# Optimization experiments

Measured on AMD Instinct MI355X. Metric: run time of the kernel, lower is better.

Reference implementation:

```python
import jax, jax.numpy as jnp
import numpy as np

N_NODES = 50000
N_EDGES = 600000
IN_FEAT = 128
OUT_FEAT = 128
NUM_RELS = 8


def setup_inputs() -> dict:
    key = jax.random.key(0)
    ks = jax.random.split(key, 8)
    h = jax.random.normal(ks[0], (N_NODES, IN_FEAT), dtype=jnp.float32)
    # xavier_uniform-like scale for relation weights
    limit = float(np.sqrt(6.0 / (IN_FEAT + OUT_FEAT)))
    weight = jax.random.uniform(ks[1], (NUM_RELS, IN_FEAT, OUT_FEAT), jnp.float32, -limit, limit)
    limit_g = float(np.sqrt(6.0 / (IN_FEAT + 1)))
    gate_weight = jax.random.uniform(ks[2], (NUM_RELS, IN_FEAT, 1), jnp.float32, -limit_g, limit_g)
    h_bias = jnp.zeros((OUT_FEAT,), jnp.float32)
    loop_weight = jax.random.uniform(ks[3], (IN_FEAT, OUT_FEAT), jnp.float32, -limit, limit)
    norm = jax.random.uniform(ks[4], (N_EDGES, 1), jnp.float32)
    src = jax.random.randint(ks[5], (N_EDGES,), 0, N_NODES, dtype=jnp.int32)
    dst = jax.random.randint(ks[6], (N_EDGES,), 0, N_NODES, dtype=jnp.int32)
    rel_type = jax.random.randint(ks[7], (N_EDGES,), 0, NUM_RELS, dtype=jnp.int32)
    return {"h": h, "weight": weight, "gate_weight": gate_weight, "h_bias": h_bias,
            "loop_weight": loop_weight, "norm": norm, "src": src, "dst": dst,
            "rel_type": rel_type}


def reference(h, weight, gate_weight, h_bias, loop_weight, norm, src, dst, rel_type):
    n_nodes = h.shape[0]
    # Transform all nodes under every relation once ([R, N, out]); cheaper than
    # materializing per-edge [E, in, out] weight gathers for small R.
    h_rel = jnp.einsum('ni,rio->rno', h, weight)          # [R, N, out]
    msg = h_rel[rel_type, src]                             # [E, out] gather
    msg = msg * norm                                       # per-edge norm
    # relation-specific scalar gate on src features
    gate_rel = jnp.einsum('ni,ri->rn', h, gate_weight[:, :, 0])  # [R, N]
    gate = jax.nn.sigmoid(gate_rel[rel_type, src])[:, None]      # [E, 1]
    msg = msg * gate
    # scatter-sum messages into destination nodes
    agg = jax.ops.segment_sum(msg, dst, num_segments=n_nodes)    # [N, out]
    out = agg + h_bias + h @ loop_weight                   # bias + self-loop
    out = jax.nn.relu(out)                                 # activation
    # dropout p=0.0 (deterministic) -> identity
    return out
```

## Files before the change

kernel.cpp:

```cpp
#include <hip/hip_runtime.h>

#define N_NODES 50000
#define N_EDGES 600000
#define F 128
#define NRELL 9
#define NB_SCAN 196

#define WT_OFF     0
#define WT_BYTES   (9*128*128*2)
#define GATE_OFF   294912
#define GATE_BYTES (8*N_NODES*4)
#define HREL_OFF   1894912
#define HREL_BYTES (9ll*N_NODES*128*2)
#define CNT_OFF    117094912
#define BASE_OFF   117294912
#define CUR_OFF    117494912
#define BSUM_OFF   117694912
#define SORT_OFF   117695936
#define WS_NEED2   ((size_t)120095936)
#define WS_NEED1   ((size_t)HREL_OFF + (size_t)HREL_BYTES)

typedef __attribute__((ext_vector_type(8))) short short8;
typedef __attribute__((ext_vector_type(4))) float floatx4;

__device__ inline unsigned short f32_to_bf16(float f) {
    unsigned u = __float_as_uint(f);
    unsigned r = u + 0x7fff + ((u >> 16) & 1);
    return (unsigned short)(r >> 16);
}
__device__ inline float bf16_to_f32(unsigned short s) {
    return __uint_as_float(((unsigned)s) << 16);
}
__device__ inline float sigmoidf(float x) { return 1.f / (1.f + __expf(-x)); }

__global__ void k_prep_w(const float* __restrict__ W, const float* __restrict__ LW,
                         unsigned short* __restrict__ Wt) {
    int idx = blockIdx.x * 256 + threadIdx.x;
    if (idx >= 9 * 128 * 128) return;
    int r = idx >> 14;
    int rem = idx & 16383;
    int i = rem >> 7, o = rem & 127;
    float v = (r < 8) ? W[(r << 14) + (i << 7) + o] : LW[(i << 7) + o];
    Wt[(r << 14) + (o << 7) + i] = f32_to_bf16(v);
}

__global__ void k_gate(const float* __restrict__ h, const float* __restrict__ gw,
                       float* __restrict__ gate) {
    int wave = threadIdx.x >> 6, lane = threadIdx.x & 63;
    int n = blockIdx.x * 4 + wave;
    if (n >= N_NODES) return;
    float2 hv = *(const float2*)(h + (size_t)n * F + lane * 2);
    #pragma unroll
    for (int r = 0; r < 8; ++r) {
        float2 wv = *(const float2*)(gw + r * F + lane * 2);
        float p = hv.x * wv.x + hv.y * wv.y;
        #pragma unroll
        for (int off = 32; off; off >>= 1) p += __shfl_xor(p, off);
        if (lane == 0) gate[r * N_NODES + n] = sigmoidf(p);
    }
}

#define LDH 136
#define LDW 136
__global__ __launch_bounds__(256) void k_hrel(const float* __restrict__ h,
                                              const unsigned short* __restrict__ Wt,
                                              unsigned short* __restrict__ hrel) {
    __shared__ unsigned short hA[64 * LDH];
    __shared__ unsigned short wB[128 * LDW];
    int tid = threadIdx.x;
    int nb = blockIdx.x * 64;

    #pragma unroll
    for (int it = 0; it < 8; ++it) {
        int idx = it * 1024 + tid * 4;
        int row = idx >> 7, col = idx & 127;
        int node = nb + row;
        float4 v;
        if (node < N_NODES) v = *(const float4*)(h + (size_t)node * F + col);
        else                v = make_float4(0.f, 0.f, 0.f, 0.f);
        ushort4 b;
        b.x = f32_to_bf16(v.x); b.y = f32_to_bf16(v.y);
        b.z = f32_to_bf16(v.z); b.w = f32_to_bf16(v.w);
        *(ushort4*)(&hA[row * LDH + col]) = b;
    }

    int wave = tid >> 6, lane = tid & 63;
    int lrow = lane & 15, quad = lane >> 4;
    const unsigned short* aptr = &hA[(wave * 16 + lrow) * LDH + quad * 8];

    for (int r = 0; r < NRELL; ++r) {
        __syncthreads();
        #pragma unroll
        for (int it = 0; it < 8; ++it) {
            int idx = it * 2048 + tid * 8;
            int o = idx >> 7, i = idx & 127;
            *(uint4*)(&wB[o * LDW + i]) = *(const uint4*)(Wt + (r << 14) + idx);
        }
        __syncthreads();

        floatx4 acc[8];
        #pragma unroll
        for (int nt = 0; nt < 8; ++nt) acc[nt] = (floatx4){0.f, 0.f, 0.f, 0.f};
        #pragma unroll
        for (int kt = 0; kt < 4; ++kt) {
            short8 a = *(const short8*)(aptr + kt * 32);
            #pragma unroll
            for (int nt = 0; nt < 8; ++nt) {
                short8 b = *(const short8*)(&wB[(nt * 16 + lrow) * LDW + kt * 32 + quad * 8]);
                acc[nt] = __builtin_amdgcn_mfma_f32_16x16x32_bf16(a, b, acc[nt], 0, 0, 0);
            }
        }
        unsigned short* dstp = hrel + (size_t)r * N_NODES * F;
        #pragma unroll
        for (int nt = 0; nt < 8; ++nt) {
            #pragma unroll
            for (int g = 0; g < 4; ++g) {
                int node = nb + wave * 16 + quad * 4 + g;
                if (node < N_NODES)
                    dstp[(size_t)node * F + nt * 16 + lrow] = f32_to_bf16(acc[nt][g]);
            }
        }
    }
}

__global__ void k_hist(const int* __restrict__ dst, int* __restrict__ cnt) {
    int e = blockIdx.x * 256 + threadIdx.x;
    if (e < N_EDGES) atomicAdd(&cnt[dst[e]], 1);
}

__global__ void k_scan1(const int* __restrict__ cnt, int* __restrict__ excl,
                        int* __restrict__ bsum) {
    __shared__ int sh[256];
    int g = blockIdx.x * 256 + threadIdx.x;
    int v = (g < N_NODES) ? cnt[g] : 0;
    sh[threadIdx.x] = v;
    __syncthreads();
    #pragma unroll
    for (int off = 1; off < 256; off <<= 1) {
        int t = (threadIdx.x >= off) ? sh[threadIdx.x - off] : 0;
        __syncthreads();
        sh[threadIdx.x] += t;
        __syncthreads();
    }
    if (g < N_NODES) excl[g] = sh[threadIdx.x] - v;
    if (threadIdx.x == 255) bsum[blockIdx.x] = sh[255];
}

__global__ void k_scan2(int* __restrict__ bsum) {
    __shared__ int sh[256];
    int v = (threadIdx.x < NB_SCAN) ? bsum[threadIdx.x] : 0;
    sh[threadIdx.x] = v;
    __syncthreads();
    #pragma unroll
    for (int off = 1; off < 256; off <<= 1) {
        int t = (threadIdx.x >= off) ? sh[threadIdx.x - off] : 0;
        __syncthreads();
        sh[threadIdx.x] += t;
        __syncthreads();
    }
    if (threadIdx.x < NB_SCAN) bsum[threadIdx.x] = sh[threadIdx.x] - v;
}

__global__ void k_scan3(int* __restrict__ excl, const int* __restrict__ bsum,
                        int* __restrict__ cursor) {
    int g = blockIdx.x * 256 + threadIdx.x;
    if (g < N_NODES) {
        int b = excl[g] + bsum[blockIdx.x];
        excl[g] = b;
        cursor[g] = b;
    }
}

__global__ void k_scatter(const int* __restrict__ dst, int* __restrict__ cursor,
                          int* __restrict__ sorted) {
    int e = blockIdx.x * 256 + threadIdx.x;
    if (e < N_EDGES) {
        int pos = atomicAdd(&cursor[dst[e]], 1);
        sorted[pos] = e;
    }
}

__global__ __launch_bounds__(256) void k_agg(const unsigned short* __restrict__ hrel,
                      const float* __restrict__ gate,
                      const float* __restrict__ norm,
                      const int* __restrict__ src, const int* __restrict__ rel,
                      const int* __restrict__ sorted,
                      const int* __restrict__ base, const int* __restrict__ cnt,
                      const float* __restrict__ bias,
                      float* __restrict__ out) {
    int wave = threadIdx.x >> 6, lane = threadIdx.x & 63;
    int n = blockIdx.x * 4 + wave;
    if (n >= N_NODES) return;
    int startp = base[n];
    int deg = cnt[n];
    float acc0 = 0.f, acc1 = 0.f;
    for (int c0 = 0; c0 < deg; c0 += 64) {
        int myi = c0 + lane;
        float sc = 0.f;
        int row = 0;
        if (myi < deg) {
            int e = sorted[startp + myi];
            int s = src[e], r = rel[e];
            row = r * N_NODES + s;
            sc = norm[e] * gate[row];
        }
        int lim = (deg - c0 < 64) ? (deg - c0) : 64;
        for (int i = 0; i < lim; ++i) {
            float scl = __shfl(sc, i);
            int rw = __shfl(row, i);
            unsigned m = *(const unsigned*)(hrel + (size_t)rw * F + lane * 2);
            acc0 += scl * bf16_to_f32((unsigned short)(m & 0xffffu));
            acc1 += scl * bf16_to_f32((unsigned short)(m >> 16));
        }
    }
    const unsigned short* hrel8 = hrel + (size_t)8 * N_NODES * F;
    unsigned l8 = *(const unsigned*)(hrel8 + (size_t)n * F + lane * 2);
    float2 bv = *(const float2*)(bias + lane * 2);
    float o0 = fmaxf(acc0 + bv.x + bf16_to_f32((unsigned short)(l8 & 0xffffu)), 0.f);
    float o1 = fmaxf(acc1 + bv.y + bf16_to_f32((unsigned short)(l8 >> 16)), 0.f);
    *(float2*)(out + (size_t)n * F + lane * 2) = make_float2(o0, o1);
}

__global__ void k_edges(const unsigned short* __restrict__ hrel,
                        const float* __restrict__ gate,
                        const float* __restrict__ norm,
                        const int* __restrict__ src, const int* __restrict__ dst,
                        const int* __restrict__ rel,
                        float* __restrict__ out) {
    int wave = threadIdx.x >> 6, lane = threadIdx.x & 63;
    int e = blockIdx.x * 4 + wave;
    if (e >= N_EDGES) return;
    int s = src[e], d = dst[e], r = rel[e];
    float scale = norm[e] * gate[r * N_NODES + s];
    unsigned int m = *(const unsigned int*)(hrel + ((size_t)r * N_NODES + s) * F + lane * 2);
    float v0 = bf16_to_f32((unsigned short)(m & 0xffffu)) * scale;
    float v1 = bf16_to_f32((unsigned short)(m >> 16)) * scale;
    float* op = out + (size_t)d * F + lane * 2;
    unsafeAtomicAdd(op, v0);
    unsafeAtomicAdd(op + 1, v1);
}

__global__ void k_final(float* __restrict__ out, const float* __restrict__ bias,
                        const unsigned short* __restrict__ hrel8) {
    int idx = blockIdx.x * 256 + threadIdx.x;
    if (idx >= N_NODES * 32) return;
    int node = idx >> 5, c4 = (idx & 31) * 4;
    float4 a = *(float4*)(out + (size_t)node * F + c4);
    float4 b = *(const float4*)(bias + c4);
    ushort4 l = *(const ushort4*)(hrel8 + (size_t)node * F + c4);
    float o0 = fmaxf(a.x + b.x + bf16_to_f32(l.x), 0.f);
    float o1 = fmaxf(a.y + b.y + bf16_to_f32(l.y), 0.f);
    float o2 = fmaxf(a.z + b.z + bf16_to_f32(l.z), 0.f);
    float o3 = fmaxf(a.w + b.w + bf16_to_f32(l.w), 0.f);
    *(float4*)(out + (size_t)node * F + c4) = make_float4(o0, o1, o2, o3);
}

__global__ void k_edges_fb(const float* __restrict__ h, const float* __restrict__ W,
                           const float* __restrict__ gw, const float* __restrict__ norm,
                           const int* __restrict__ src, const int* __restrict__ dst,
                           const int* __restrict__ rel, float* __restrict__ out) {
    int wave = threadIdx.x >> 6, lane = threadIdx.x & 63;
    int e = blockIdx.x * 4 + wave;
    if (e >= N_EDGES) return;
    int s = src[e], d = dst[e], r = rel[e];
    float2 hv = *(const float2*)(h + (size_t)s * F + lane * 2);
    float2 gv = *(const float2*)(gw + r * F + lane * 2);
    float p = hv.x * gv.x + hv.y * gv.y;
    #pragma unroll
    for (int off = 32; off; off >>= 1) p += __shfl_xor(p, off);
    float scale = norm[e] * sigmoidf(p);
    const float* wr = W + ((size_t)r << 14);
    float a0 = 0.f, a1 = 0.f;
    for (int i2 = 0; i2 < 64; ++i2) {
        float x0 = __shfl(hv.x, i2), x1 = __shfl(hv.y, i2);
        a0 += x0 * wr[(2 * i2) * F + lane]      + x1 * wr[(2 * i2 + 1) * F + lane];
        a1 += x0 * wr[(2 * i2) * F + 64 + lane] + x1 * wr[(2 * i2 + 1) * F + 64 + lane];
    }
    unsafeAtomicAdd(out + (size_t)d * F + lane,      a0 * scale);
    unsafeAtomicAdd(out + (size_t)d * F + 64 + lane, a1 * scale);
}

__global__ void k_final_fb(const float* __restrict__ h, const float* __restrict__ LW,
                           const float* __restrict__ bias, float* __restrict__ out) {
    int wave = threadIdx.x >> 6, lane = threadIdx.x & 63;
    int n = blockIdx.x * 4 + wave;
    if (n >= N_NODES) return;
    float2 hv = *(const float2*)(h + (size_t)n * F + lane * 2);
    float a0 = 0.f, a1 = 0.f;
    for (int i2 = 0; i2 < 64; ++i2) {
        float x0 = __shfl(hv.x, i2), x1 = __shfl(hv.y, i2);
        a0 += x0 * LW[(2 * i2) * F + lane]      + x1 * LW[(2 * i2 + 1) * F + lane];
        a1 += x0 * LW[(2 * i2) * F + 64 + lane] + x1 * LW[(2 * i2 + 1) * F + 64 + lane];
    }
    float* op = out + (size_t)n * F;
    op[lane]      = fmaxf(op[lane]      + bias[lane]      + a0, 0.f);
    op[64 + lane] = fmaxf(op[64 + lane] + bias[64 + lane] + a1, 0.f);
}

extern "C" void kernel_launch(void* const* d_in, const int* in_sizes, int n_in,
                              void* d_out, int out_size, void* d_ws, size_t ws_size,
                              hipStream_t stream) {
    const float* h    = (const float*)d_in[0];
    const float* W    = (const float*)d_in[1];
    const float* gw   = (const float*)d_in[2];
    const float* bias = (const float*)d_in[3];
    const float* lw   = (const float*)d_in[4];
    const float* norm = (const float*)d_in[5];
    const int* src    = (const int*)d_in[6];
    const int* dst    = (const int*)d_in[7];
    const int* rel    = (const int*)d_in[8];
    float* out = (float*)d_out;

    if (ws_size >= WS_NEED2) {
        unsigned short* Wt   = (unsigned short*)d_ws;
        float*          gate = (float*)((char*)d_ws + GATE_OFF);
        unsigned short* hrel = (unsigned short*)((char*)d_ws + HREL_OFF);
        int* cnt    = (int*)((char*)d_ws + CNT_OFF);
        int* base   = (int*)((char*)d_ws + BASE_OFF);
        int* cursor = (int*)((char*)d_ws + CUR_OFF);
        int* bsum   = (int*)((char*)d_ws + BSUM_OFF);
        int* sorted = (int*)((char*)d_ws + SORT_OFF);

        hipMemsetAsync(cnt, 0, N_NODES * sizeof(int), stream);
        k_prep_w<<<576, 256, 0, stream>>>(W, lw, Wt);
        k_gate<<<12500, 256, 0, stream>>>(h, gw, gate);
        k_hist<<<2344, 256, 0, stream>>>(dst, cnt);
        k_scan1<<<NB_SCAN, 256, 0, stream>>>(cnt, base, bsum);
        k_scan2<<<1, 256, 0, stream>>>(bsum);
        k_scan3<<<NB_SCAN, 256, 0, stream>>>(base, bsum, cursor);
        k_scatter<<<2344, 256, 0, stream>>>(dst, cursor, sorted);
        k_hrel<<<782, 256, 0, stream>>>(h, Wt, hrel);
        k_agg<<<12500, 256, 0, stream>>>(hrel, gate, norm, src, rel, sorted,
                                         base, cnt, bias, out);
    } else if (ws_size >= WS_NEED1) {
        unsigned short* Wt   = (unsigned short*)d_ws;
        float*          gate = (float*)((char*)d_ws + GATE_OFF);
        unsigned short* hrel = (unsigned short*)((char*)d_ws + HREL_OFF);
        hipMemsetAsync(d_out, 0, (size_t)out_size * sizeof(float), stream);
        k_prep_w<<<576, 256, 0, stream>>>(W, lw, Wt);
        k_gate<<<12500, 256, 0, stream>>>(h, gw, gate);
        k_hrel<<<782, 256, 0, stream>>>(h, Wt, hrel);
        k_edges<<<150000, 256, 0, stream>>>(hrel, gate, norm, src, dst, rel, out);
        k_final<<<6250, 256, 0, stream>>>(out, bias, hrel + (size_t)8 * N_NODES * F);
    } else {
        hipMemsetAsync(d_out, 0, (size_t)out_size * sizeof(float), stream);
        k_edges_fb<<<150000, 256, 0, stream>>>(h, W, gw, norm, src, dst, rel, out);
        k_final_fb<<<12500, 256, 0, stream>>>(h, lw, bias, out);
    }
}
```

Before: 302.4 us.

## Aggregate raw features per relation first, then one fused GEMM over concatenated relations

Reorders the computation so messages are summed per (dst, relation) from bf16 node features first, then multiplied by the stacked relation and self-loop weights in a single K=1152 MFMA GEMM with fused bias and ReLU. This avoids materialising the 9×N×128 transformed-feature tensor and the per-edge gathers from it. Edges are bucketed by dst*8+rel, with norm×gate folded into packed (src, scale) records. The new path adds an extra bf16 rounding of the aggregates, a larger scan, and depends on a workspace of about 138 MB being available.

```diff
diff --git a/kernel.cpp b/kernel.cpp
--- a/kernel.cpp
+++ b/kernel.cpp
@@ -5,11 +5,19 @@
 #define F 128
 #define NRELL 9
 #define NB_SCAN 196
-
-#define WT_OFF     0
-#define WT_BYTES   (9*128*128*2)
+#define NB2 1563
+
+#define WT3_OFF   0
+#define H2_OFF    294912
+#define GATE3_OFF 13094912
+#define CNT3_OFF  14694912
+#define EXCL3_OFF 16294912
+#define BSUM3_OFF 17895168
+#define REC3_OFF  17901568
+#define A3_OFF    22701568
+#define WS_NEED3  ((size_t)138012160)
+
 #define GATE_OFF   294912
-#define GATE_BYTES (8*N_NODES*4)
 #define HREL_OFF   1894912
 #define HREL_BYTES (9ll*N_NODES*128*2)
 #define CNT_OFF    117094912
@@ -31,17 +39,230 @@
 __device__ inline float bf16_to_f32(unsigned short s) {
     return __uint_as_float(((unsigned)s) << 16);
 }
+__device__ inline float bf16lo(unsigned m) { return __uint_as_float(m << 16); }
+__device__ inline float bf16hi(unsigned m) { return __uint_as_float(m & 0xffff0000u); }
 __device__ inline float sigmoidf(float x) { return 1.f / (1.f + __expf(-x)); }
 
 __global__ void k_prep_w(const float* __restrict__ W, const float* __restrict__ LW,
-                         unsigned short* __restrict__ Wt) {
+                         unsigned short* __restrict__ Wt, int swz) {
     int idx = blockIdx.x * 256 + threadIdx.x;
     if (idx >= 9 * 128 * 128) return;
     int r = idx >> 14;
     int rem = idx & 16383;
     int i = rem >> 7, o = rem & 127;
     float v = (r < 8) ? W[(r << 14) + (i << 7) + o] : LW[(i << 7) + o];
-    Wt[(r << 14) + (o << 7) + i] = f32_to_bf16(v);
+    int pos;
+    if (swz) {
+        int g = (i >> 3) ^ (o & 7);
+        pos = (r << 14) + (o << 7) + (g << 3) + (i & 7);
+    } else {
+        pos = (r << 14) + (o << 7) + i;
+    }
+    Wt[pos] = f32_to_bf16(v);
+}
+
+__global__ void k_prep_h(const float* __restrict__ h, const float* __restrict__ gw,
+                         unsigned short* __restrict__ h2, float* __restrict__ gate) {
+    int wave = threadIdx.x >> 6, lane = threadIdx.x & 63;
+    int n = blockIdx.x * 4 + wave;
+    float2 hv = *(const float2*)(h + (size_t)n * F + lane * 2);
+    unsigned val = (unsigned)f32_to_bf16(hv.x) | ((unsigned)f32_to_bf16(hv.y) << 16);
+    *(unsigned*)(h2 + (size_t)n * F + lane * 2) = val;
+    #pragma unroll
+    for (int r = 0; r < 8; ++r) {
+        float2 wv = *(const float2*)(gw + r * F + lane * 2);
+        float p = hv.x * wv.x + hv.y * wv.y;
+        #pragma unroll
+        for (int off = 32; off; off >>= 1) p += __shfl_xor(p, off);
+        if (lane == 0) gate[r * N_NODES + n] = sigmoidf(p);
+    }
+}
+
+__global__ void k_hist2(const int* __restrict__ dst, const int* __restrict__ rel,
+                        int* __restrict__ cnt) {
+    int e = blockIdx.x * 256 + threadIdx.x;
+    if (e < N_EDGES) atomicAdd(&cnt[dst[e] * 8 + rel[e]], 1);
+}
+
+__global__ void k_s1(const int* __restrict__ cnt, int* __restrict__ excl,
+                     int* __restrict__ bsum) {
+    __shared__ int sh[256];
+    int g = blockIdx.x * 256 + threadIdx.x;
+    int v = (g < 400000) ? cnt[g] : 0;
+    sh[threadIdx.x] = v;
+    __syncthreads();
+    #pragma unroll
+    for (int off = 1; off < 256; off <<= 1) {
+        int t = (threadIdx.x >= off) ? sh[threadIdx.x - off] : 0;
+        __syncthreads();
+        sh[threadIdx.x] += t;
+        __syncthreads();
+    }
+    if (g < 400000) excl[g] = sh[threadIdx.x] - v;
+    if (threadIdx.x == 255) bsum[blockIdx.x] = sh[255];
+}
+
+__global__ void k_s2(int* __restrict__ bsum) {
+    __shared__ int sh[256];
+    int t = threadIdx.x;
+    int v[7];
+    int s = 0;
+    #pragma unroll
+    for (int j = 0; j < 7; ++j) {
+        int idx = t * 7 + j;
+        v[j] = (idx < NB2) ? bsum[idx] : 0;
+        s += v[j];
+    }
+    sh[t] = s;
+    __syncthreads();
+    #pragma unroll
+    for (int off = 1; off < 256; off <<= 1) {
+        int tt = (t >= off) ? sh[t - off] : 0;
+        __syncthreads();
+        sh[t] += tt;
+        __syncthreads();
+    }
+    int run = sh[t] - s;
+    #pragma unroll
+    for (int j = 0; j < 7; ++j) {
+        int idx = t * 7 + j;
+        if (idx < NB2) bsum[idx] = run;
+        run += v[j];
+    }
+}
+
+__global__ void k_s3(int* __restrict__ excl, const int* __restrict__ bsum,
+                     int* __restrict__ cursor) {
+    int g = blockIdx.x * 256 + threadIdx.x;
+    if (g < 400000) {
+        int b = excl[g] + bsum[blockIdx.x];
+        excl[g] = b;
+        cursor[g] = b;
+    }
+    if (g == 0) excl[400000] = N_EDGES;
+}
+
+__global__ void k_scatter2(const int* __restrict__ src, const int* __restrict__ dst,
+                           const int* __restrict__ rel, const float* __restrict__ norm,
+                           const float* __restrict__ gate, int* __restrict__ cursor,
+                           int2* __restrict__ rec) {
+    int e = blockIdx.x * 256 + threadIdx.x;
+    if (e >= N_EDGES) return;
+    int d = dst[e], r = rel[e], s = src[e];
+    int pos = atomicAdd(&cursor[d * 8 + r], 1);
+    float sc = norm[e] * gate[r * N_NODES + s];
+    rec[pos] = make_int2(s, __float_as_int(sc));
+}
+
+__global__ __launch_bounds__(256) void k_aggA(const unsigned short* __restrict__ h2,
+                                              const int2* __restrict__ rec,
+                                              const int* __restrict__ excl,
+                                              unsigned short* __restrict__ A) {
+    int wave = threadIdx.x >> 6, lane = threadIdx.x & 63;
+    int n = blockIdx.x * 4 + wave;
+    int ex = 0;
+    if (lane < 9) ex = excl[n * 8 + lane];
+    int e0 = __shfl(ex, 0), e8 = __shfl(ex, 8);
+    int deg = e8 - e0;
+    unsigned short* Arow = A + (size_t)n * 1152;
+    int swo = (((lane >> 2) ^ (n & 7)) << 2) + (lane & 3);
+
+    if (deg <= 64) {
+        int rs = 0; float rsc = 0.f;
+        if (lane < deg) {
+            int2 rc = rec[e0 + lane];
+            rs = rc.x; rsc = __int_as_float(rc.y);
+        }
+        for (int r = 0; r < 8; ++r) {
+            int s = __shfl(ex, r) - e0;
+            int e = __shfl(ex, r + 1) - e0;
+            float a0 = 0.f, a1 = 0.f;
+            for (int j = s; j < e; ++j) {
+                int sj = __shfl(rs, j);
+                float sc = __shfl(rsc, j);
+                unsigned m = *(const unsigned*)(h2 + (size_t)sj * F + lane * 2);
+                a0 += sc * bf16lo(m);
+                a1 += sc * bf16hi(m);
+            }
+            unsigned val = (unsigned)f32_to_bf16(a0) | ((unsigned)f32_to_bf16(a1) << 16);
+            ((unsigned*)(Arow + r * 128))[swo] = val;
+        }
+    } else {
+        for (int r = 0; r < 8; ++r) {
+            int s = __shfl(ex, r);
+            int e = __shfl(ex, r + 1);
+            float a0 = 0.f, a1 = 0.f;
+            for (int idx = s; idx < e; ++idx) {
+                int2 rc = rec[idx];
+                float sc = __int_as_float(rc.y);
+                unsigned m = *(const unsigned*)(h2 + (size_t)rc.x * F + lane * 2);
+                a0 += sc * bf16lo(m);
+                a1 += sc * bf16hi(m);
+            }
+            unsigned val = (unsigned)f32_to_bf16(a0) | ((unsigned)f32_to_bf16(a1) << 16);
+            ((unsigned*)(Arow + r * 128))[swo] = val;
+        }
+    }
+    unsigned hm = ((const unsigned*)(h2 + (size_t)n * F))[lane];
+    ((unsigned*)(Arow + 8 * 128))[swo] = hm;
+}
+
+__global__ __launch_bounds__(256) void k_gemmA(const unsigned short* __restrict__ A,
+                                               const unsigned short* __restrict__ Wt,
+                                               const float* __restrict__ bias,
+                                               float* __restrict__ out) {
+    __shared__ unsigned short sA[16384];
+    __shared__ unsigned short sB[16384];
+    int tid = threadIdx.x;
+    int nb = blockIdx.x * 128;
+    int wave = tid >> 6, lane = tid & 63, lrow = lane & 15, quad = lane >> 4;
+
+    floatx4 acc[2][8];
+    #pragma unroll
+    for (int mt = 0; mt < 2; ++mt)
+        #pragma unroll
+        for (int nt = 0; nt < 8; ++nt) acc[mt][nt] = (floatx4){0.f, 0.f, 0.f, 0.f};
+
+    for (int kb = 0; kb < 9; ++kb) {
+        __syncthreads();
+        #pragma unroll
+        for (int it = 0; it < 8; ++it) {
+            int g = it * 256 + tid;
+            int row = g >> 4, gr = g & 15;
+            *(uint4*)(&sA[row * 128 + gr * 8]) =
+                *(const uint4*)(A + (size_t)(nb + row) * 1152 + kb * 128 + gr * 8);
+            *(uint4*)(&sB[row * 128 + gr * 8]) =
+                *(const uint4*)(Wt + (kb << 14) + (g << 3));
+        }
+        __syncthreads();
+        #pragma unroll
+        for (int kt = 0; kt < 4; ++kt) {
+            int j = kt * 4 + quad;
+            int sw = (j ^ (lrow & 7)) << 3;
+            short8 a0 = *(const short8*)(&sA[(wave * 32 + lrow) * 128 + sw]);
+            short8 a1 = *(const short8*)(&sA[(wave * 32 + 16 + lrow) * 128 + sw]);
+            #pragma unroll
+            for (int nt = 0; nt < 8; ++nt) {
+                short8 b = *(const short8*)(&sB[(nt * 16 + lrow) * 128 + sw]);
+                acc[0][nt] = __builtin_amdgcn_mfma_f32_16x16x32_bf16(a0, b, acc[0][nt], 0, 0, 0);
+                acc[1][nt] = __builtin_amdgcn_mfma_f32_16x16x32_bf16(a1, b, acc[1][nt], 0, 0, 0);
+            }
+        }
+    }
+    #pragma unroll
+    for (int mt = 0; mt < 2; ++mt) {
+        #pragma unroll
+        for (int nt = 0; nt < 8; ++nt) {
+            int col = nt * 16 + lrow;
+            float bv = bias[col];
+            #pragma unroll
+            for (int g = 0; g < 4; ++g) {
+                int row = nb + wave * 32 + mt * 16 + quad * 4 + g;
+                if (row < N_NODES)
+                    out[(size_t)row * F + col] = fmaxf(acc[mt][nt][g] + bv, 0.f);
+            }
+        }
+    }
 }
 
 __global__ void k_gate(const float* __restrict__ h, const float* __restrict__ gw,
@@ -69,7 +290,6 @@
     __shared__ unsigned short wB[128 * LDW];
     int tid = threadIdx.x;
     int nb = blockIdx.x * 64;
-
     #pragma unroll
     for (int it = 0; it < 8; ++it) {
         int idx = it * 1024 + tid * 4;
@@ -83,11 +303,9 @@
         b.z = f32_to_bf16(v.z); b.w = f32_to_bf16(v.w);
         *(ushort4*)(&hA[row * LDH + col]) = b;
     }
-
     int wave = tid >> 6, lane = tid & 63;
     int lrow = lane & 15, quad = lane >> 4;
     const unsigned short* aptr = &hA[(wave * 16 + lrow) * LDH + quad * 8];
-
     for (int r = 0; r < NRELL; ++r) {
         __syncthreads();
         #pragma unroll
@@ -97,7 +315,6 @@
             *(uint4*)(&wB[o * LDW + i]) = *(const uint4*)(Wt + (r << 14) + idx);
         }
         __syncthreads();
-
         floatx4 acc[8];
         #pragma unroll
         for (int nt = 0; nt < 8; ++nt) acc[nt] = (floatx4){0.f, 0.f, 0.f, 0.f};
@@ -209,15 +426,15 @@
             float scl = __shfl(sc, i);
             int rw = __shfl(row, i);
             unsigned m = *(const unsigned*)(hrel + (size_t)rw * F + lane * 2);
-            acc0 += scl * bf16_to_f32((unsigned short)(m & 0xffffu));
-            acc1 += scl * bf16_to_f32((unsigned short)(m >> 16));
+            acc0 += scl * bf16lo(m);
+            acc1 += scl * bf16hi(m);
         }
     }
     const unsigned short* hrel8 = hrel + (size_t)8 * N_NODES * F;
     unsigned l8 = *(const unsigned*)(hrel8 + (size_t)n * F + lane * 2);
     float2 bv = *(const float2*)(bias + lane * 2);
-    float o0 = fmaxf(acc0 + bv.x + bf16_to_f32((unsigned short)(l8 & 0xffffu)), 0.f);
-    float o1 = fmaxf(acc1 + bv.y + bf16_to_f32((unsigned short)(l8 >> 16)), 0.f);
+    float o0 = fmaxf(acc0 + bv.x + bf16lo(l8), 0.f);
+    float o1 = fmaxf(acc1 + bv.y + bf16hi(l8), 0.f);
     *(float2*)(out + (size_t)n * F + lane * 2) = make_float2(o0, o1);
 }
 
@@ -233,8 +450,8 @@
     int s = src[e], d = dst[e], r = rel[e];
     float scale = norm[e] * gate[r * N_NODES + s];
     unsigned int m = *(const unsigned int*)(hrel + ((size_t)r * N_NODES + s) * F + lane * 2);
-    float v0 = bf16_to_f32((unsigned short)(m & 0xffffu)) * scale;
-    float v1 = bf16_to_f32((unsigned short)(m >> 16)) * scale;
+    float v0 = bf16lo(m) * scale;
+    float v1 = bf16hi(m) * scale;
     float* op = out + (size_t)d * F + lane * 2;
     unsafeAtomicAdd(op, v0);
     unsafeAtomicAdd(op + 1, v1);
@@ -311,7 +528,27 @@
     const int* rel    = (const int*)d_in[8];
     float* out = (float*)d_out;
 
-    if (ws_size >= WS_NEED2) {
+    if (ws_size >= WS_NEED3) {
+        unsigned short* Wt   = (unsigned short*)((char*)d_ws + WT3_OFF);
+        unsigned short* h2   = (unsigned short*)((char*)d_ws + H2_OFF);
+        float*          gate = (float*)((char*)d_ws + GATE3_OFF);
+        int*            cnt  = (int*)((char*)d_ws + CNT3_OFF);
+        int*            excl = (int*)((char*)d_ws + EXCL3_OFF);
+        int*            bsum = (int*)((char*)d_ws + BSUM3_OFF);
+        int2*           rec  = (int2*)((char*)d_ws + REC3_OFF);
+        unsigned short* A    = (unsigned short*)((char*)d_ws + A3_OFF);
+
+        hipMemsetAsync(cnt, 0, 400000 * sizeof(int), stream);
+        k_prep_w<<<576, 256, 0, stream>>>(W, lw, Wt, 1);
+        k_prep_h<<<12500, 256, 0, stream>>>(h, gw, h2, gate);
+        k_hist2<<<2344, 256, 0, stream>>>(dst, rel, cnt);
+        k_s1<<<NB2, 256, 0, stream>>>(cnt, excl, bsum);
+        k_s2<<<1, 256, 0, stream>>>(bsum);
+        k_s3<<<NB2, 256, 0, stream>>>(excl, bsum, cnt);
+        k_scatter2<<<2344, 256, 0, stream>>>(src, dst, rel, norm, gate, cnt, rec);
+        k_aggA<<<12500, 256, 0, stream>>>(h2, rec, excl, A);
+        k_gemmA<<<391, 256, 0, stream>>>(A, Wt, bias, out);
+    } else if (ws_size >= WS_NEED2) {
         unsigned short* Wt   = (unsigned short*)d_ws;
         float*          gate = (float*)((char*)d_ws + GATE_OFF);
         unsigned short* hrel = (unsigned short*)((char*)d_ws + HREL_OFF);
@@ -320,9 +557,8 @@
         int* cursor = (int*)((char*)d_ws + CUR_OFF);
         int* bsum   = (int*)((char*)d_ws + BSUM_OFF);
         int* sorted = (int*)((char*)d_ws + SORT_OFF);
-
         hipMemsetAsync(cnt, 0, N_NODES * sizeof(int), stream);
-        k_prep_w<<<576, 256, 0, stream>>>(W, lw, Wt);
+        k_prep_w<<<576, 256, 0, stream>>>(W, lw, Wt, 0);
         k_gate<<<12500, 256, 0, stream>>>(h, gw, gate);
         k_hist<<<2344, 256, 0, stream>>>(dst, cnt);
         k_scan1<<<NB_SCAN, 256, 0, stream>>>(cnt, base, bsum);
@@ -337,7 +573,7 @@
         float*          gate = (float*)((char*)d_ws + GATE_OFF);
         unsigned short* hrel = (unsigned short*)((char*)d_ws + HREL_OFF);
         hipMemsetAsync(d_out, 0, (size_t)out_size * sizeof(float), stream);
-        k_prep_w<<<576, 256, 0, stream>>>(W, lw, Wt);
+        k_prep_w<<<576, 256, 0, stream>>>(W, lw, Wt, 0);
         k_gate<<<12500, 256, 0, stream>>>(h, gw, gate);
         k_hrel<<<782, 256, 0, stream>>>(h, Wt, hrel);
         k_edges<<<150000, 256, 0, stream>>>(hrel, gate, norm, src, dst, rel, out);
```

After: 272.1 us. 10.0% less time.
